# Kernel optimization log

Measured on AMD Instinct MI355X. Metric: run time of the kernel, lower is better.

The kernel has to match this reference:

```python
import jax, jax.numpy as jnp
import numpy as np
from jax import lax

B, H, W, C = 16, 256, 256, 1
LOC_C = 31            # channels out of localization network
BN_EPS = 1e-3         # Keras BatchNormalization default epsilon
NEG_SLOPE = 0.1       # LeakyReLU slope


def _conv_relu(x, k, b):
    y = lax.conv_general_dilated(x, k, (1, 1), 'SAME',
                                 dimension_numbers=('NHWC', 'HWIO', 'NHWC'))
    return jax.nn.relu(y + b)


def _maxpool2(x):
    return lax.reduce_window(x, -jnp.inf, lax.max, (1, 2, 2, 1), (1, 2, 2, 1), 'VALID')


def _resize_nearest(x, out_h, out_w):
    # tf.image.resize(..., method='nearest') with half-pixel centers
    b, h, w, c = x.shape
    ih = jnp.floor((jnp.arange(out_h) + 0.5) * h / out_h).astype(jnp.int32)
    iw = jnp.floor((jnp.arange(out_w) + 0.5) * w / out_w).astype(jnp.int32)
    return x[:, ih][:, :, iw]


def _generate_grid(theta, height, width):
    # base grid in [-1, 1], x varies along width, y along height
    xs = jnp.arange(width, dtype=jnp.float32) / (width - 1) * 2.0 - 1.0
    ys = jnp.arange(height, dtype=jnp.float32) / (height - 1) * 2.0 - 1.0
    gx, gy = jnp.meshgrid(xs, ys)                      # (H, W)
    grid = jnp.stack([gx, gy], axis=-1).reshape(height * width, 2)  # (HW, 2)
    th = theta.reshape(-1, 2, 3)
    A = th[:, :, :2]                                   # (B, 2, 2)
    t = th[:, :, 2]                                    # (B, 2)
    # NOTE: source does grid @ A (not A @ grid) -- replicate exactly
    tg = jnp.einsum('nc,bcd->bnd', grid, A) + t[:, None, :]
    return tg.reshape(-1, height, width, 2)


def _sampler(img, grid):
    b, h, w, c = img.shape
    x = 0.5 * ((grid[..., 0] + 1.0) * (w - 1))
    y = 0.5 * ((grid[..., 1] + 1.0) * (h - 1))
    x0 = jnp.floor(x); x1 = x0 + 1.0
    y0 = jnp.floor(y); y1 = y0 + 1.0
    x0 = jnp.clip(x0, 0.0, w - 1.0); x1 = jnp.clip(x1, 0.0, w - 1.0)
    y0 = jnp.clip(y0, 0.0, h - 1.0); y1 = jnp.clip(y1, 0.0, h - 1.0)
    wa = (x1 - x) * (y1 - y)
    wb = (x1 - x) * (y - y0)
    wc = (x - x0) * (y1 - y)
    wd = (x - x0) * (y - y0)
    xi0 = x0.astype(jnp.int32); xi1 = x1.astype(jnp.int32)
    yi0 = y0.astype(jnp.int32); yi1 = y1.astype(jnp.int32)
    img_flat = img.reshape(b, h * w, c)

    def gather(yi, xi):
        idx = (yi * w + xi).reshape(b, h * w, 1)       # (B, HW, 1)
        return jnp.take_along_axis(img_flat, idx, axis=1).reshape(b, h, w, c)

    Ia = gather(yi0, xi0)
    Ib = gather(yi1, xi0)
    Ic = gather(yi0, xi1)
    Id = gather(yi1, xi1)
    return (wa[..., None] * Ia + wb[..., None] * Ib
            + wc[..., None] * Ic + wd[..., None] * Id)


def setup_inputs() -> dict:
    key = jax.random.key(0)
    ks = jax.random.split(key, 16)
    s = 0.05
    feat = (H // 8) * (W // 8) * LOC_C  # 31744 flattened localization features
    return {
        'x': jax.random.normal(ks[0], (B, H, W, C), jnp.float32),
        'conv1_k': jax.random.normal(ks[1], (3, 3, C, 8), jnp.float32) * s,
        'conv1_b': jnp.zeros((8,), jnp.float32),
        'conv2_k': jax.random.normal(ks[2], (3, 3, 8, 16), jnp.float32) * s,
        'conv2_b': jnp.zeros((16,), jnp.float32),
        'conv3_k': jax.random.normal(ks[3], (3, 3, 16, LOC_C), jnp.float32) * s,
        'conv3_b': jnp.zeros((LOC_C,), jnp.float32),
        'bn_gamma': 1.0 + 0.1 * jax.random.normal(ks[4], (feat,), jnp.float32),
        'bn_beta': 0.1 * jax.random.normal(ks[5], (feat,), jnp.float32),
        'bn_mean': jnp.zeros((feat,), jnp.float32),
        'bn_var': jnp.ones((feat,), jnp.float32),
        'd1_k': jax.random.normal(ks[6], (feat, 64), jnp.float32) * 0.01,
        'd1_b': jnp.zeros((64,), jnp.float32),
        'd2_k': jax.random.normal(ks[7], (64, 96), jnp.float32) * s,
        'd2_b': jnp.zeros((96,), jnp.float32),
        'd3_k': jax.random.normal(ks[8], (96, 6), jnp.float32) * 0.01,
        'd3_b': jnp.array([1, 0, 0, 0, 1, 0], jnp.float32),
    }


def reference(x, conv1_k, conv1_b, conv2_k, conv2_b, conv3_k, conv3_b,
              bn_gamma, bn_beta, bn_mean, bn_var,
              d1_k, d1_b, d2_k, d2_b, d3_k, d3_b):
    # localization network: (conv-relu, pool) x3 -> (B, H/8, W/8, 31)
    xi = _maxpool2(_conv_relu(x, conv1_k, conv1_b))
    xi = _maxpool2(_conv_relu(xi, conv2_k, conv2_b))
    x_intermediate = _maxpool2(_conv_relu(xi, conv3_k, conv3_b))
    # transformation parameter network (BN in inference mode, dropout = identity)
    f = x_intermediate.reshape(x.shape[0], -1)
    f = (f - bn_mean) * jax.lax.rsqrt(bn_var + BN_EPS) * bn_gamma + bn_beta
    f = jax.nn.relu(f @ d1_k + d1_b)
    f = jax.nn.relu(f @ d2_k + d2_b)
    theta = f @ d3_k + d3_b                            # (B, 6)
    grid = _generate_grid(theta, H, W)                 # (B, H, W, 2)
    loc_up = _resize_nearest(x_intermediate, H, W)     # (B, H, W, 31)
    xc = jnp.concatenate([x, loc_up], axis=-1)         # (B, H, W, 32)
    out = _sampler(xc, grid)
    return jnp.where(out >= 0, out, NEG_SLOPE * out)
```

## Files before the change

kernel.cpp:

```cpp
#include <hip/hip_runtime.h>


#define NEG_SLOPE 0.1f
#define BN_EPS 1e-3f

typedef float vfloat4 __attribute__((ext_vector_type(4)));

__device__ __forceinline__ void fma4v(float pv, float4 wq, float* __restrict__ acc) {
    acc[0] = fmaf(pv, wq.x, acc[0]);
    acc[1] = fmaf(pv, wq.y, acc[1]);
    acc[2] = fmaf(pv, wq.z, acc[2]);
    acc[3] = fmaf(pv, wq.w, acc[3]);
}

__global__ __launch_bounds__(256) void st_conv1(const float* __restrict__ x,
                                                const float* __restrict__ w,
                                                const float* __restrict__ bias,
                                                float* __restrict__ outA) {
    int idx = blockIdx.x * 256 + threadIdx.x;
    int px = idx & 127, py = (idx >> 7) & 127, b = idx >> 14;
    const float* xb = x + b * 65536;
    int iy0 = 2 * py - 1, ix0 = 2 * px - 1;
    float p[16];
#pragma unroll
    for (int r = 0; r < 4; ++r) {
        int iy = iy0 + r;
        bool oky = (iy >= 0) && (iy < 256);
#pragma unroll
        for (int cc = 0; cc < 4; ++cc) {
            int ix = ix0 + cc;
            bool ok = oky && (ix >= 0) && (ix < 256);
            p[r * 4 + cc] = ok ? xb[iy * 256 + ix] : 0.0f;
        }
    }
    float m[8];
#pragma unroll
    for (int co = 0; co < 8; ++co) m[co] = -1e30f;
#pragma unroll
    for (int oy = 0; oy < 2; ++oy)
#pragma unroll
        for (int ox = 0; ox < 2; ++ox) {
            float acc[8];
#pragma unroll
            for (int co = 0; co < 8; ++co) acc[co] = 0.0f;
#pragma unroll
            for (int ky = 0; ky < 3; ++ky)
#pragma unroll
                for (int kx = 0; kx < 3; ++kx) {
                    float pv = p[(oy + ky) * 4 + (ox + kx)];
                    const float* wr = w + (ky * 3 + kx) * 8;
#pragma unroll
                    for (int co = 0; co < 8; ++co)
                        acc[co] = fmaf(pv, wr[co], acc[co]);
                }
#pragma unroll
            for (int co = 0; co < 8; ++co) m[co] = fmaxf(m[co], acc[co]);
        }
    float4 o0, o1;
    float r0 = m[0] + bias[0], r1 = m[1] + bias[1], r2 = m[2] + bias[2], r3 = m[3] + bias[3];
    float r4 = m[4] + bias[4], r5 = m[5] + bias[5], r6 = m[6] + bias[6], r7 = m[7] + bias[7];
    o0.x = r0 > 0.f ? r0 : 0.f; o0.y = r1 > 0.f ? r1 : 0.f;
    o0.z = r2 > 0.f ? r2 : 0.f; o0.w = r3 > 0.f ? r3 : 0.f;
    o1.x = r4 > 0.f ? r4 : 0.f; o1.y = r5 > 0.f ? r5 : 0.f;
    o1.z = r6 > 0.f ? r6 : 0.f; o1.w = r7 > 0.f ? r7 : 0.f;
    *(float4*)(outA + idx * 8) = o0;
    *(float4*)(outA + idx * 8 + 4) = o1;
}

__global__ __launch_bounds__(256) void st_conv2(const float* __restrict__ A,
                                                const float* __restrict__ w,
                                                const float* __restrict__ bias,
                                                float* __restrict__ outB) {
    __shared__ __align__(16) float wlds[1152];
    int t = threadIdx.x;
    for (int i = t; i < 1152; i += 256) wlds[i] = w[i];
    __syncthreads();
    int lane = t & 63;
    int wv = __builtin_amdgcn_readfirstlane(t >> 6);
    int cobase = wv * 4;
    int pixel = blockIdx.x * 64 + lane;
    int px = pixel & 63, py = (pixel >> 6) & 63, b = pixel >> 12;
    const float* Ab = A + b * 128 * 128 * 8;
    int iy0 = 2 * py - 1, ix0 = 2 * px - 1;
    float acc[4][4];
#pragma unroll
    for (int pos = 0; pos < 4; ++pos)
#pragma unroll
        for (int c = 0; c < 4; ++c) acc[pos][c] = 0.0f;

#pragma unroll 1
    for (int ciq = 0; ciq < 2; ++ciq) {
        float ps[64];
#pragma unroll
        for (int r = 0; r < 4; ++r) {
            int iy = iy0 + r;
            bool oky = (iy >= 0) && (iy < 128);
#pragma unroll
            for (int cc = 0; cc < 4; ++cc) {
                int ix = ix0 + cc;
                bool ok = oky && (ix >= 0) && (ix < 128);
                float4 v = ok ? *(const float4*)(Ab + ((iy * 128 + ix) * 8 + ciq * 4))
                              : float4{0.f, 0.f, 0.f, 0.f};
                int cell = r * 4 + cc;
                ps[cell * 4 + 0] = v.x; ps[cell * 4 + 1] = v.y;
                ps[cell * 4 + 2] = v.z; ps[cell * 4 + 3] = v.w;
            }
        }
#pragma unroll
        for (int ky = 0; ky < 3; ++ky)
#pragma unroll
            for (int kx = 0; kx < 3; ++kx) {
                int tap = ky * 3 + kx;
#pragma unroll
                for (int comp = 0; comp < 4; ++comp) {
                    float4 wq = *(const float4*)&wlds[((tap * 8 + ciq * 4 + comp) << 4) + cobase];
#pragma unroll
                    for (int oy = 0; oy < 2; ++oy)
#pragma unroll
                        for (int ox = 0; ox < 2; ++ox) {
                            float pv = ps[((oy + ky) * 4 + (ox + kx)) * 4 + comp];
                            fma4v(pv, wq, acc[oy * 2 + ox]);
                        }
                }
            }
    }
    float4 o;
    float* oc = (float*)&o;
#pragma unroll
    for (int c = 0; c < 4; ++c) {
        float m = fmaxf(fmaxf(acc[0][c], acc[1][c]), fmaxf(acc[2][c], acc[3][c]));
        m += bias[cobase + c];
        oc[c] = m > 0.0f ? m : 0.0f;
    }
    *(float4*)(outB + pixel * 16 + cobase) = o;
}

__global__ __launch_bounds__(256) void st_conv3p(const float* __restrict__ Bf,
                                                 const float* __restrict__ w,
                                                 const float* __restrict__ bias,
                                                 const float* __restrict__ gamma,
                                                 const float* __restrict__ beta,
                                                 const float* __restrict__ mean,
                                                 const float* __restrict__ var,
                                                 float* __restrict__ xip,
                                                 float* __restrict__ fprime) {
    __shared__ __align__(16) float wlds[9 * 16 * 32];
    int t = threadIdx.x;
    for (int i = t; i < 4464; i += 256) {
        int tapci = i / 31;
        int co = i - tapci * 31;
        wlds[(tapci << 5) + co] = w[i];
    }
    __syncthreads();
    int lane = t & 63;
    int wv = __builtin_amdgcn_readfirstlane(t >> 6);
    int quad = blockIdx.y * 4 + wv;
    int cobase = quad * 4;
    if (cobase > 27) cobase = 27;
    int pixel = blockIdx.x * 64 + lane;
    int b = pixel >> 10;
    int cell = pixel & 1023;
    int ppy = cell >> 5, ppx = cell & 31;
    const float* Bb = Bf + b * 64 * 64 * 16;
    int iy0 = 2 * ppy - 1, ix0 = 2 * ppx - 1;
    float acc[4][4];
#pragma unroll
    for (int pos = 0; pos < 4; ++pos)
#pragma unroll
        for (int c = 0; c < 4; ++c) acc[pos][c] = 0.0f;

#pragma unroll 1
    for (int ciq = 0; ciq < 4; ++ciq) {
        float ps[64];
#pragma unroll
        for (int r = 0; r < 4; ++r) {
            int y = iy0 + r;
            bool oky = (y >= 0) && (y < 64);
#pragma unroll
            for (int cc = 0; cc < 4; ++cc) {
                int xx = ix0 + cc;
                bool ok = oky && (xx >= 0) && (xx < 64);
                float4 v = ok ? *(const float4*)(Bb + ((y * 64 + xx) * 16 + ciq * 4))
                              : float4{0.f, 0.f, 0.f, 0.f};
                int cell2 = r * 4 + cc;
                ps[cell2 * 4 + 0] = v.x; ps[cell2 * 4 + 1] = v.y;
                ps[cell2 * 4 + 2] = v.z; ps[cell2 * 4 + 3] = v.w;
            }
        }
#pragma unroll
        for (int ky = 0; ky < 3; ++ky)
#pragma unroll
            for (int kx = 0; kx < 3; ++kx) {
                int tap = ky * 3 + kx;
#pragma unroll
                for (int comp = 0; comp < 4; ++comp) {
                    float4 wq = *(const float4*)&wlds[((tap * 16 + ciq * 4 + comp) << 5) + cobase];
#pragma unroll
                    for (int oy = 0; oy < 2; ++oy)
#pragma unroll
                        for (int ox = 0; ox < 2; ++ox) {
                            float pv = ps[((oy + ky) * 4 + (ox + kx)) * 4 + comp];
                            fma4v(pv, wq, acc[oy * 2 + ox]);
                        }
                }
            }
    }
    float* xcell = xip + (b << 15) + (cell << 5) + 1 + cobase;
#pragma unroll
    for (int c = 0; c < 4; ++c) {
        float m = fmaxf(fmaxf(acc[0][c], acc[1][c]), fmaxf(acc[2][c], acc[3][c]));
        m += bias[cobase + c];
        float v = m > 0.0f ? m : 0.0f;
        xcell[c] = v;
        int j = cell * 31 + cobase + c;
        float sc = gamma[j] * rsqrtf(var[j] + BN_EPS);
        fprime[j * 16 + b] = (v - mean[j]) * sc + beta[j];
    }
}

__global__ __launch_bounds__(256) void st_d1(const float* __restrict__ fp,
                                             const float* __restrict__ k1,
                                             float* __restrict__ partial) {
    int t = threadIdx.x, s = blockIdx.x;
    int o = t & 63;
    int sub = t >> 6;
    int subu = __builtin_amdgcn_readfirstlane(sub);
    int j0 = s * 124 + subu * 31;
    float acc[16];
#pragma unroll
    for (int b = 0; b < 16; ++b) acc[b] = 0.0f;
    for (int jj = 0; jj < 31; ++jj) {
        int j = j0 + jj;
        float kv = k1[j * 64 + o];
        const float* fpj = fp + j * 16;
#pragma unroll
        for (int b = 0; b < 16; ++b)
            acc[b] = fmaf(fpj[b], kv, acc[b]);
    }
    __shared__ float red[4][16][64];
#pragma unroll
    for (int b = 0; b < 16; ++b) red[sub][b][o] = acc[b];
    __syncthreads();
    if (sub == 0) {
#pragma unroll
        for (int b = 0; b < 16; ++b) {
            float v = red[0][b][o] + red[1][b][o] + red[2][b][o] + red[3][b][o];
            partial[(s * 64 + o) * 16 + b] = v;
        }
    }
}

__global__ __launch_bounds__(256) void st_d1b(const float* __restrict__ partial,
                                              const float* __restrict__ bias,
                                              float* __restrict__ h1) {
    int gid = blockIdx.x * 256 + threadIdx.x;
    int o = gid >> 4, b = gid & 15;
    float s = 0.0f;
#pragma unroll 8
    for (int sl = 0; sl < 256; ++sl) s += partial[(sl * 64 + o) * 16 + b];
    s += bias[o];
    h1[b * 64 + o] = s > 0.0f ? s : 0.0f;
}

__global__ __launch_bounds__(128) void st_theta(const float* __restrict__ h1,
                                                const float* __restrict__ k2,
                                                const float* __restrict__ b2,
                                                const float* __restrict__ k3,
                                                const float* __restrict__ b3,
                                                float* __restrict__ theta) {
    int b = blockIdx.x, t = threadIdx.x;
    __shared__ float h2[96];
    if (t < 96) {
        float s = b2[t];
        for (int i = 0; i < 64; ++i) s = fmaf(h1[b * 64 + i], k2[i * 96 + t], s);
        h2[t] = s > 0.0f ? s : 0.0f;
    }
    __syncthreads();
    if (t < 6) {
        float s = b3[t];
        for (int i = 0; i < 96; ++i) s = fmaf(h2[i], k3[i * 6 + t], s);
        theta[b * 6 + t] = s;
    }
}

__global__ __launch_bounds__(256) void st_sample(const float* __restrict__ x,
                                                 const float* __restrict__ xip,
                                                 const float* __restrict__ theta,
                                                 float* __restrict__ out) {
    int gid = blockIdx.x * 256 + threadIdx.x;
    int q = gid & 3;
    int pix = gid >> 2;
    int ow = pix & 255, oh = (pix >> 8) & 255;
    int b = __builtin_amdgcn_readfirstlane(blockIdx.x >> 10);

    const float* th = theta + b * 6;
    float t0 = th[0], t1 = th[1], t2 = th[2], t3 = th[3], t4 = th[4], t5 = th[5];
    float gx = (float)ow * (2.0f / 255.0f) - 1.0f;
    float gy = (float)oh * (2.0f / 255.0f) - 1.0f;
    float sx = gx * t0 + gy * t3 + t2;
    float sy = gx * t1 + gy * t4 + t5;
    float xf = 0.5f * ((sx + 1.0f) * 255.0f);
    float yf = 0.5f * ((sy + 1.0f) * 255.0f);
    float x0 = floorf(xf), y0 = floorf(yf);
    float x1 = x0 + 1.0f, y1 = y0 + 1.0f;
    x0 = fminf(fmaxf(x0, 0.0f), 255.0f);
    x1 = fminf(fmaxf(x1, 0.0f), 255.0f);
    y0 = fminf(fmaxf(y0, 0.0f), 255.0f);
    y1 = fminf(fmaxf(y1, 0.0f), 255.0f);
    float wa = (x1 - xf) * (y1 - yf);
    float wb = (x1 - xf) * (yf - y0);
    float wc = (xf - x0) * (y1 - yf);
    float wd = (xf - x0) * (yf - y0);
    int xi0 = (int)x0, xi1 = (int)x1, yi0 = (int)y0, yi1 = (int)y1;

    const float* cellbase = xip + (b << 15);
    int off = q * 8;
    const float* pa = cellbase + ((((yi0 >> 3) << 5) + (xi0 >> 3)) << 5) + off;
    const float* pb = cellbase + ((((yi1 >> 3) << 5) + (xi0 >> 3)) << 5) + off;
    const float* pc = cellbase + ((((yi0 >> 3) << 5) + (xi1 >> 3)) << 5) + off;
    const float* pd = cellbase + ((((yi1 >> 3) << 5) + (xi1 >> 3)) << 5) + off;

    float r[8];
#pragma unroll
    for (int k = 0; k < 2; ++k) {
        float4 va = *(const float4*)(pa + 4 * k);
        float4 vb = *(const float4*)(pb + 4 * k);
        float4 vc = *(const float4*)(pc + 4 * k);
        float4 vd = *(const float4*)(pd + 4 * k);
        r[4 * k]     = fmaf(wa, va.x, fmaf(wb, vb.x, fmaf(wc, vc.x, wd * vd.x)));
        r[4 * k + 1] = fmaf(wa, va.y, fmaf(wb, vb.y, fmaf(wc, vc.y, wd * vd.y)));
        r[4 * k + 2] = fmaf(wa, va.z, fmaf(wb, vb.z, fmaf(wc, vc.z, wd * vd.z)));
        r[4 * k + 3] = fmaf(wa, va.w, fmaf(wb, vb.w, fmaf(wc, vc.w, wd * vd.w)));
    }
    if (q == 0) {
        const float* xb = x + b * 65536;
        float Ia = xb[yi0 * 256 + xi0];
        float Ib = xb[yi1 * 256 + xi0];
        float Ic = xb[yi0 * 256 + xi1];
        float Id = xb[yi1 * 256 + xi1];
        r[0] = fmaf(wa, Ia, fmaf(wb, Ib, fmaf(wc, Ic, wd * Id)));
    }
#pragma unroll
    for (int i = 0; i < 8; ++i) r[i] = r[i] >= 0.0f ? r[i] : NEG_SLOPE * r[i];

    float* ob = out + pix * 32 + off;
    vfloat4 v0 = {r[0], r[1], r[2], r[3]};
    vfloat4 v1 = {r[4], r[5], r[6], r[7]};
    __builtin_nontemporal_store(v0, (vfloat4*)ob);
    __builtin_nontemporal_store(v1, (vfloat4*)(ob + 4));
}

extern "C" void kernel_launch(void* const* d_in, const int* in_sizes, int n_in,
                              void* d_out, int out_size, void* d_ws, size_t ws_size,
                              hipStream_t stream) {
    const float* x     = (const float*)d_in[0];
    const float* c1k   = (const float*)d_in[1];
    const float* c1b   = (const float*)d_in[2];
    const float* c2k   = (const float*)d_in[3];
    const float* c2b   = (const float*)d_in[4];
    const float* c3k   = (const float*)d_in[5];
    const float* c3b   = (const float*)d_in[6];
    const float* gamma = (const float*)d_in[7];
    const float* beta  = (const float*)d_in[8];
    const float* mean  = (const float*)d_in[9];
    const float* var   = (const float*)d_in[10];
    const float* d1k   = (const float*)d_in[11];
    const float* d1b   = (const float*)d_in[12];
    const float* d2k   = (const float*)d_in[13];
    const float* d2b   = (const float*)d_in[14];
    const float* d3k   = (const float*)d_in[15];
    const float* d3b   = (const float*)d_in[16];
    float* out = (float*)d_out;
    float* ws  = (float*)d_ws;

    float* A       = ws;
    float* Bf      = ws + 2097152;
    float* xip     = ws;
    float* fprime  = ws + 524288;
    float* partial = ws + 3145728;
    float* h1      = ws + 3407872;
    float* theta   = ws + 3408896;

    st_conv1<<<1024, 256, 0, stream>>>(x, c1k, c1b, A);
    st_conv2<<<1024, 256, 0, stream>>>(A, c2k, c2b, Bf);
    st_conv3p<<<dim3(256, 2), 256, 0, stream>>>(Bf, c3k, c3b, gamma, beta,
                                                mean, var, xip, fprime);
    st_d1<<<256, 256, 0, stream>>>(fprime, d1k, partial);
    st_d1b<<<4, 256, 0, stream>>>(partial, d1b, h1);
    st_theta<<<16, 128, 0, stream>>>(h1, d2k, d2b, d3k, d3b, theta);
    st_sample<<<16384, 256, 0, stream>>>(x, xip, theta, out);
}
```

Before: 265.9 us.

## Pad conv intermediates with zero halos and split dense-1 reduction wider

Conv1 and conv2 now write their outputs into buffers padded with a one-pixel zero border, and conv1 also zeroes those borders. This lets conv2 and conv3 load their 4x4 input windows without per-element bounds checks, and their channel loops are unrolled more. The first dense layer's split-K reduction uses 496 slices of 16 rows instead of 256 slices of 31, giving more blocks in parallel, and the second stage reduces over more partial sums. In exchange the padded buffers are slightly larger and the partial-sum buffer is bigger.

```diff
diff --git a/kernel.cpp b/kernel.cpp
--- a/kernel.cpp
+++ b/kernel.cpp
@@ -16,7 +16,8 @@
 __global__ __launch_bounds__(256) void st_conv1(const float* __restrict__ x,
                                                 const float* __restrict__ w,
                                                 const float* __restrict__ bias,
-                                                float* __restrict__ outA) {
+                                                float* __restrict__ Ap,
+                                                float* __restrict__ Bp) {
     int idx = blockIdx.x * 256 + threadIdx.x;
     int px = idx & 127, py = (idx >> 7) & 127, b = idx >> 14;
     const float* xb = x + b * 65536;
@@ -63,14 +64,38 @@
     o0.z = r2 > 0.f ? r2 : 0.f; o0.w = r3 > 0.f ? r3 : 0.f;
     o1.x = r4 > 0.f ? r4 : 0.f; o1.y = r5 > 0.f ? r5 : 0.f;
     o1.z = r6 > 0.f ? r6 : 0.f; o1.w = r7 > 0.f ? r7 : 0.f;
-    *(float4*)(outA + idx * 8) = o0;
-    *(float4*)(outA + idx * 8 + 4) = o1;
-}
-
-__global__ __launch_bounds__(256) void st_conv2(const float* __restrict__ A,
+    float* o = Ap + ((b * 130 + py + 1) * 130 + (px + 1)) * 8;
+    *(float4*)o = o0;
+    *(float4*)(o + 4) = o1;
+
+    const float4 z4 = {0.f, 0.f, 0.f, 0.f};
+    if (idx < 8256) {
+        int bb = idx / 516, t = idx - bb * 516;
+        int iy, ix;
+        if (t < 130)      { iy = 0;       ix = t; }
+        else if (t < 260) { iy = 129;     ix = t - 130; }
+        else if (t < 388) { iy = t - 259; ix = 0; }
+        else              { iy = t - 387; ix = 129; }
+        float* d = Ap + ((bb * 130 + iy) * 130 + ix) * 8;
+        *(float4*)d = z4; *(float4*)(d + 4) = z4;
+    } else if (idx < 12416) {
+        int r = idx - 8256;
+        int bb = r / 260, t = r - bb * 260;
+        int iy, ix;
+        if (t < 66)       { iy = 0;       ix = t; }
+        else if (t < 132) { iy = 65;      ix = t - 66; }
+        else if (t < 196) { iy = t - 131; ix = 0; }
+        else              { iy = t - 195; ix = 65; }
+        float* d = Bp + ((bb * 66 + iy) * 66 + ix) * 16;
+        *(float4*)d = z4; *(float4*)(d + 4) = z4;
+        *(float4*)(d + 8) = z4; *(float4*)(d + 12) = z4;
+    }
+}
+
+__global__ __launch_bounds__(256) void st_conv2(const float* __restrict__ Ap,
                                                 const float* __restrict__ w,
                                                 const float* __restrict__ bias,
-                                                float* __restrict__ outB) {
+                                                float* __restrict__ Bp) {
     __shared__ __align__(16) float wlds[1152];
     int t = threadIdx.x;
     for (int i = t; i < 1152; i += 256) wlds[i] = w[i];
@@ -80,32 +105,26 @@
     int cobase = wv * 4;
     int pixel = blockIdx.x * 64 + lane;
     int px = pixel & 63, py = (pixel >> 6) & 63, b = pixel >> 12;
-    const float* Ab = A + b * 128 * 128 * 8;
-    int iy0 = 2 * py - 1, ix0 = 2 * px - 1;
+    const float* Ab = Ap + b * 135200;
+    int rowbase = (2 * py) * 130 + 2 * px;
     float acc[4][4];
 #pragma unroll
     for (int pos = 0; pos < 4; ++pos)
 #pragma unroll
         for (int c = 0; c < 4; ++c) acc[pos][c] = 0.0f;
 
-#pragma unroll 1
+#pragma unroll
     for (int ciq = 0; ciq < 2; ++ciq) {
         float ps[64];
 #pragma unroll
-        for (int r = 0; r < 4; ++r) {
-            int iy = iy0 + r;
-            bool oky = (iy >= 0) && (iy < 128);
+        for (int r = 0; r < 4; ++r)
 #pragma unroll
             for (int cc = 0; cc < 4; ++cc) {
-                int ix = ix0 + cc;
-                bool ok = oky && (ix >= 0) && (ix < 128);
-                float4 v = ok ? *(const float4*)(Ab + ((iy * 128 + ix) * 8 + ciq * 4))
-                              : float4{0.f, 0.f, 0.f, 0.f};
+                float4 v = *(const float4*)(Ab + (rowbase + r * 130 + cc) * 8 + ciq * 4);
                 int cell = r * 4 + cc;
                 ps[cell * 4 + 0] = v.x; ps[cell * 4 + 1] = v.y;
                 ps[cell * 4 + 2] = v.z; ps[cell * 4 + 3] = v.w;
             }
-        }
 #pragma unroll
         for (int ky = 0; ky < 3; ++ky)
 #pragma unroll
@@ -132,10 +151,10 @@
         m += bias[cobase + c];
         oc[c] = m > 0.0f ? m : 0.0f;
     }
-    *(float4*)(outB + pixel * 16 + cobase) = o;
-}
-
-__global__ __launch_bounds__(256) void st_conv3p(const float* __restrict__ Bf,
+    *(float4*)(Bp + ((b * 66 + py + 1) * 66 + (px + 1)) * 16 + cobase) = o;
+}
+
+__global__ __launch_bounds__(256) void st_conv3p(const float* __restrict__ Bp,
                                                  const float* __restrict__ w,
                                                  const float* __restrict__ bias,
                                                  const float* __restrict__ gamma,
@@ -161,32 +180,26 @@
     int b = pixel >> 10;
     int cell = pixel & 1023;
     int ppy = cell >> 5, ppx = cell & 31;
-    const float* Bb = Bf + b * 64 * 64 * 16;
-    int iy0 = 2 * ppy - 1, ix0 = 2 * ppx - 1;
+    const float* Bb = Bp + b * 69696;
+    int rowbase = (2 * ppy) * 66 + 2 * ppx;
     float acc[4][4];
 #pragma unroll
     for (int pos = 0; pos < 4; ++pos)
 #pragma unroll
         for (int c = 0; c < 4; ++c) acc[pos][c] = 0.0f;
 
-#pragma unroll 1
+#pragma unroll 2
     for (int ciq = 0; ciq < 4; ++ciq) {
         float ps[64];
 #pragma unroll
-        for (int r = 0; r < 4; ++r) {
-            int y = iy0 + r;
-            bool oky = (y >= 0) && (y < 64);
+        for (int r = 0; r < 4; ++r)
 #pragma unroll
             for (int cc = 0; cc < 4; ++cc) {
-                int xx = ix0 + cc;
-                bool ok = oky && (xx >= 0) && (xx < 64);
-                float4 v = ok ? *(const float4*)(Bb + ((y * 64 + xx) * 16 + ciq * 4))
-                              : float4{0.f, 0.f, 0.f, 0.f};
+                float4 v = *(const float4*)(Bb + (rowbase + r * 66 + cc) * 16 + ciq * 4);
                 int cell2 = r * 4 + cc;
                 ps[cell2 * 4 + 0] = v.x; ps[cell2 * 4 + 1] = v.y;
                 ps[cell2 * 4 + 2] = v.z; ps[cell2 * 4 + 3] = v.w;
             }
-        }
 #pragma unroll
         for (int ky = 0; ky < 3; ++ky)
 #pragma unroll
@@ -225,11 +238,12 @@
     int o = t & 63;
     int sub = t >> 6;
     int subu = __builtin_amdgcn_readfirstlane(sub);
-    int j0 = s * 124 + subu * 31;
+    int j0 = s * 64 + subu * 16;
     float acc[16];
 #pragma unroll
     for (int b = 0; b < 16; ++b) acc[b] = 0.0f;
-    for (int jj = 0; jj < 31; ++jj) {
+#pragma unroll 4
+    for (int jj = 0; jj < 16; ++jj) {
         int j = j0 + jj;
         float kv = k1[j * 64 + o];
         const float* fpj = fp + j * 16;
@@ -257,7 +271,7 @@
     int o = gid >> 4, b = gid & 15;
     float s = 0.0f;
 #pragma unroll 8
-    for (int sl = 0; sl < 256; ++sl) s += partial[(sl * 64 + o) * 16 + b];
+    for (int sl = 0; sl < 496; ++sl) s += partial[(sl * 64 + o) * 16 + b];
     s += bias[o];
     h1[b * 64 + o] = s > 0.0f ? s : 0.0f;
 }
@@ -373,19 +387,19 @@
     float* out = (float*)d_out;
     float* ws  = (float*)d_ws;
 
-    float* A       = ws;
-    float* Bf      = ws + 2097152;
+    float* Ap      = ws;
+    float* Bp      = ws + 2163200;
     float* xip     = ws;
     float* fprime  = ws + 524288;
-    float* partial = ws + 3145728;
-    float* h1      = ws + 3407872;
-    float* theta   = ws + 3408896;
-
-    st_conv1<<<1024, 256, 0, stream>>>(x, c1k, c1b, A);
-    st_conv2<<<1024, 256, 0, stream>>>(A, c2k, c2b, Bf);
-    st_conv3p<<<dim3(256, 2), 256, 0, stream>>>(Bf, c3k, c3b, gamma, beta,
+    float* partial = ws + 3278336;
+    float* h1      = ws + 3786240;
+    float* theta   = ws + 3787264;
+
+    st_conv1<<<1024, 256, 0, stream>>>(x, c1k, c1b, Ap, Bp);
+    st_conv2<<<1024, 256, 0, stream>>>(Ap, c2k, c2b, Bp);
+    st_conv3p<<<dim3(256, 2), 256, 0, stream>>>(Bp, c3k, c3b, gamma, beta,
                                                 mean, var, xip, fprime);
-    st_d1<<<256, 256, 0, stream>>>(fprime, d1k, partial);
+    st_d1<<<496, 256, 0, stream>>>(fprime, d1k, partial);
     st_d1b<<<4, 256, 0, stream>>>(partial, d1b, h1);
     st_theta<<<16, 128, 0, stream>>>(h1, d2k, d2b, d3k, d3b, theta);
     st_sample<<<16384, 256, 0, stream>>>(x, xip, theta, out);
```

After: 263.3 us. Within noise of the previous version (-1.0%).
